# Optimization experiments

Hardware: AMD Instinct MI355X
Metric: run time of the kernel (lower is better)

The kernel has to match this reference:

```python
import jax, jax.numpy as jnp
import numpy as np
from jax import lax

NEG_INF = -1e30
GAP_OPEN = -5.0
GAP_EXTEND = -1.0
TEMP = 1.0


def setup_inputs() -> dict:
    key = jax.random.key(0)
    x = jax.random.normal(key, (2048, 2048), dtype=jnp.float32)
    return {"x": x}


def _sw_forward(x):
    xin = x[:-1, :-1]
    A, B = xin.shape  # static
    ar = jnp.arange(A - 1, -1, -1)[:, None]  # (A,1)
    br = jnp.arange(B)[None, :]              # (1,B)
    i = br - ar + (A - 1)                    # (A,B) diagonal index
    j = (ar + br) // 2                       # (A,B) position within diagonal
    n = A + B - 1
    m = (A + B) // 2
    # rotate score matrix into anti-diagonal (wavefront) layout
    smx = jnp.full((n, m), NEG_INF, dtype=x.dtype).at[i, j].set(xin)
    smo = (((jnp.arange(n) + A % 2) % 2)).astype(x.dtype)  # parity per diagonal

    right_pen = jnp.array([GAP_OPEN, GAP_EXTEND, GAP_OPEN], dtype=x.dtype)   # penalize_turns
    down_pen = jnp.array([GAP_OPEN, GAP_OPEN, GAP_EXTEND], dtype=x.dtype)

    def lse(a):
        return TEMP * jax.nn.logsumexp(a / TEMP, axis=-1)

    def step(carry, inp):
        h2, h1 = carry            # each (m,3)
        sx, so = inp              # (m,), scalar
        align = jnp.pad(h2, ((0, 0), (0, 1))) + sx[:, None]  # (m,4)
        right = so * jnp.pad(h1[:-1], ((1, 0), (0, 0)), constant_values=NEG_INF) + (1.0 - so) * h1
        down = so * h1 + (1.0 - so) * jnp.pad(h1[1:], ((0, 1), (0, 0)), constant_values=NEG_INF)
        right = (right + right_pen)[:, :2]  # restrict_turns
        down = down + down_pen
        h0 = jnp.stack([lse(align), lse(right), lse(down)], axis=-1)  # (m,3)
        return (h1, h0), h0

    carry0 = (jnp.full((m, 3), NEG_INF, dtype=x.dtype),
              jnp.full((m, 3), NEG_INF, dtype=x.dtype))
    _, results = lax.scan(step, carry0, (smx, smo))  # (n,m,3)

    hij = results[i, j]  # un-rotate -> (A,B,3)
    final = TEMP * jax.nn.logsumexp((hij + x[1:, 1:, None]) / TEMP)
    return final


def reference(x):
    return _sw_forward(x)
```

## Files before the change

kernel.cpp:

```cpp
#include <hip/hip_runtime.h>
#include <hip/hip_bf16.h>
#include <math.h>

#define NN 2048
#define TROWS 1040
#define NW 8
#define RPS 16
#define LN2 0.6931471805599453


__global__ void prep_kernel(const float* __restrict__ x, float* __restrict__ tab,
                            float* __restrict__ tabR) {
  const int c = blockIdx.x * 256 + threadIdx.x;
  const int t = blockIdx.y;
  tab[(size_t)t * NN + c] = __expf(x[(size_t)t * NN + c]);
  const int rr = 2048 - t, cc = 2048 - c;
  float v = 0.f;
  if (rr < 2048 && cc < 2048) v = __expf(x[(size_t)rr * NN + cc]);
  tabR[(size_t)t * NN + c] = v;
}

template<int MODE>
__global__ __launch_bounds__(NW * 64)
void sw2_kernel(const float* __restrict__ x, const float* __restrict__ tab,
                const float* __restrict__ tabR, float* __restrict__ arr,
                float* __restrict__ out) {
  const int tid  = threadIdx.x;
  const int lane = tid & 63;
  const int wv   = __builtin_amdgcn_readfirstlane(tid >> 6);
  const int c0   = (wv << 8) + lane * 4;

  __shared__ float2 E[2][NW + 1][RPS];
  __shared__ float  red[2][NW];
  __shared__ float  wsum[NW];

  for (int i = tid; i < 2 * (NW + 1) * RPS; i += NW * 64)
    ((float2*)E)[i] = make_float2(0.f, 0.f);
  __syncthreads();

  const float cGO = 0.006737946999085467f;
  const float cGE = 0.36787944117144233f;
  const float C4  = 0.01831563888873418f;
  const bool isL0 = (lane == 0), isL1 = (lane == 1), isL63 = (lane == 63);

  if (MODE == 0 || blockIdx.x == 0) {
    const int SPW   = (MODE == 0) ? 128 : 64;
    const int NSTEP = SPW + NW - 1;
    float s1_0=0.f,s1_1=0.f,s1_2=0.f,s1_3=0.f;
    float tg0=0.f,tg1=0.f,tg2=0.f,tg3=0.f;
    float yc0=0.f,yc1=0.f,yc2=0.f,yc3=0.f;
    float acc=0.f, one=1.f, tmx=0.f, escale=1.f, SinC=0.f;
    int Etot = 0;
    const float* src = ((MODE == 0) ? x : tab) + c0;
    float4 pfA = *(const float4*)(src);
    float4 pfB = *(const float4*)(src + NN);
    const float* pl = src + 2 * NN;
    int rown = 2;

    for (int s = 0; s < NSTEP; ++s) {
      const int pr = s & 1, cr = pr ^ 1;
      const bool act = (s >= wv) && (s < wv + SPW);
      if (act) {
        float prevEdx = 0.f;
        #pragma unroll
        for (int k = 0; k < RPS; ++k) {
          float4 ev;
          if (k & 1) { ev = pfB;
            if (MODE == 1) { pfB = *(const float4*)pl; pl += NN; }
            else { int rr = (rown < NN) ? rown : NN - 1; pfB = *(const float4*)(src + (size_t)rr * NN); rown++; }
          } else { ev = pfA;
            if (MODE == 1) { pfA = *(const float4*)pl; pl += NN; }
            else { int rr = (rown < NN) ? rown : NN - 1; pfA = *(const float4*)(src + (size_t)rr * NN); rown++; }
          }
          float ex0 = ev.x, ex1 = ev.y, ex2 = ev.z, ex3 = ev.w;
          if (MODE == 0) { ex0 = __expf(ex0); ex1 = __expf(ex1); ex2 = __expf(ex2); ex3 = __expf(ex3); }

          const float2 edc = E[cr][wv][k];
          const float Sr = (k == 0) ? SinC : prevEdx * escale;
          const float Xi = edc.y * escale;
          prevEdx = edc.x;

          float sh  = __shfl_up(s1_3, 1);
          float sd0 = isL0 ? Sr : sh;
          acc = fmaf(ex0, sd0,  acc);
          acc = fmaf(ex1, s1_0, acc);
          acc = fmaf(ex2, s1_1, acc);
          acc = fmaf(ex3, s1_2, acc);
          float M0 = ex0 * (sd0  + one);
          float M1 = ex1 * (s1_0 + one);
          float M2 = ex2 * (s1_1 + one);
          float M3 = ex3 * (s1_2 + one);

          float Q  = fmaf(cGE, fmaf(cGE, fmaf(cGE, M0, M1), M2), M3);
          float q1 = __shfl_up(Q, 1);
          float q2 = __shfl_up(Q, 2);
          q2 = isL1 ? Xi : q2;
          float X0 = fmaf(C4, q2, q1);
          X0 = isL0 ? Xi : X0;
          float X1 = fmaf(cGE, X0, M0);
          float X2 = fmaf(cGE, X1, M1);
          float X3 = fmaf(cGE, X2, M2);

          float T0 = fmaf(cGO, X0, M0);
          float T1 = fmaf(cGO, X1, M1);
          float T2 = fmaf(cGO, X2, M2);
          float T3 = fmaf(cGO, X3, M3);
          float Y0 = fmaf(cGE, yc0, tg0);
          float Y1 = fmaf(cGE, yc1, tg1);
          float Y2 = fmaf(cGE, yc2, tg2);
          float Y3 = fmaf(cGE, yc3, tg3);
          float S0 = T0 + Y0, S1n = T1 + Y1, S2n = T2 + Y2, S3n = T3 + Y3;
          tmx = fmaxf(tmx, fmaxf(fmaxf(S0, S1n), fmaxf(S2n, S3n)));
          tg0 = cGO * T0; tg1 = cGO * T1; tg2 = cGO * T2; tg3 = cGO * T3;
          yc0 = Y0; yc1 = Y1; yc2 = Y2; yc3 = Y3;
          s1_0 = S0; s1_1 = S1n; s1_2 = S2n; s1_3 = S3n;

          if (isL63) E[pr][wv + 1][k] = make_float2(S3n, fmaf(C4, X0, Q));
        }
        SinC = prevEdx * escale;
      }
      {
        float m = tmx;
        m = fmaxf(m, __shfl_xor(m, 1));  m = fmaxf(m, __shfl_xor(m, 2));
        m = fmaxf(m, __shfl_xor(m, 4));  m = fmaxf(m, __shfl_xor(m, 8));
        m = fmaxf(m, __shfl_xor(m, 16)); m = fmaxf(m, __shfl_xor(m, 32));
        if (lane == 0) red[pr][wv] = m;
      }
      __syncthreads();
      {
        float mm = red[pr][lane & (NW - 1)];
        mm = fmaxf(mm, __shfl_xor(mm, 1));
        mm = fmaxf(mm, __shfl_xor(mm, 2));
        mm = fmaxf(mm, __shfl_xor(mm, 4));
        tmx = 0.f; escale = 1.f;
        int e = (mm > 0.f) ? ilogbf(mm) : 0;
        if (e > 126) e = 126; if (e < -126) e = -126;
        if (e != 0) {
          const float c = ldexpf(1.f, -e);
          s1_0*=c; s1_1*=c; s1_2*=c; s1_3*=c;
          tg0*=c; tg1*=c; tg2*=c; tg3*=c;
          yc0*=c; yc1*=c; yc2*=c; yc3*=c;
          acc*=c; one*=c; SinC*=c;
          escale = c; Etot += e;
        }
      }
    }
    float ssum = acc;
    ssum += __shfl_xor(ssum, 1);  ssum += __shfl_xor(ssum, 2);
    ssum += __shfl_xor(ssum, 4);  ssum += __shfl_xor(ssum, 8);
    ssum += __shfl_xor(ssum, 16); ssum += __shfl_xor(ssum, 32);
    if (lane == 0) wsum[wv] = ssum;
    __syncthreads();
    if (MODE == 0) {
      if (tid == 0) {
        double tot = 0.0;
        #pragma unroll
        for (int k = 0; k < NW; ++k) tot += (double)wsum[k];
        out[0] = (float)(log(tot) + (double)Etot * LN2);
      }
    } else {
      *(float4*)(arr + c0)          = make_float4(s1_0, s1_1, s1_2, s1_3);
      *(float4*)(arr + NN + c0)     = make_float4(tg0, tg1, tg2, tg3);
      *(float4*)(arr + 2 * NN + c0) = make_float4(yc0, yc1, yc2, yc3);
      if (tid == 0) {
        float t = 0.f;
        #pragma unroll
        for (int k = 0; k < NW; ++k) t += wsum[k];
        arr[5 * NN + 0] = t;
        ((int*)(arr + 5 * NN))[2] = Etot;
      }
    }
  } else {
    float gM1_0=0.f,gM1_1=0.f,gM1_2=0.f,gM1_3=0.f;
    float gY1_0=0.f,gY1_1=0.f,gY1_2=0.f,gY1_3=0.f;
    float accB=0.f, one=1.f, tmx=0.f, escale=1.f, gMinC=0.f;
    int Etot = 0;
    const float* src = tabR + c0;
    float4 pfA = *(const float4*)(src);
    float4 pfB = *(const float4*)(src + NN);
    const float* pl = src + 2 * NN;

    const int NSTEPB = 64 + NW - 1 + 1;
    for (int s = 0; s < NSTEPB; ++s) {
      const int pr = s & 1, cr = pr ^ 1;
      const bool actM = (s >= wv) && (s < wv + 64);
      const bool actE = (s == wv + 64);
      if (actM) {
        float prevEdx = 0.f;
        #pragma unroll
        for (int k = 0; k < RPS; ++k) {
          float4 ev;
          if (k & 1) { ev = pfB; pfB = *(const float4*)pl; pl += NN; }
          else       { ev = pfA; pfA = *(const float4*)pl; pl += NN; }
          const float er0 = ev.x, er1 = ev.y, er2 = ev.z, er3 = ev.w;

          const float2 edc = E[cr][wv][k];
          const float gMdIn = (k == 0) ? gMinC : prevEdx * escale;
          const float Xi = edc.y * escale;
          prevEdx = edc.x;

          float gmh  = __shfl_up(gM1_3, 1);
          float gMd0 = isL0 ? gMdIn : gmh;
          float gMd1 = gM1_0, gMd2 = gM1_1, gMd3 = gM1_2;
          accB = fmaf(er0, gMd0, accB);
          accB = fmaf(er1, gMd1, accB);
          accB = fmaf(er2, gMd2, accB);
          accB = fmaf(er3, gMd3, accB);
          float a0 = er0 * (gMd0 + one);
          float a1 = er1 * (gMd1 + one);
          float a2 = er2 * (gMd2 + one);
          float a3 = er3 * (gMd3 + one);

          float gTs0 = fmaf(cGO, gY1_0, a0);
          float gTs1 = fmaf(cGO, gY1_1, a1);
          float gTs2 = fmaf(cGO, gY1_2, a2);
          float gTs3 = fmaf(cGO, gY1_3, a3);
          float gY0n = fmaf(cGE, gY1_0, a0);
          float gY1n = fmaf(cGE, gY1_1, a1);
          float gY2n = fmaf(cGE, gY1_2, a2);
          float gY3n = fmaf(cGE, gY1_3, a3);

          float Qg = fmaf(cGE, fmaf(cGE, fmaf(cGE, gTs0, gTs1), gTs2), gTs3);
          float q1 = __shfl_up(Qg, 1);
          float q2 = __shfl_up(Qg, 2);
          q2 = isL1 ? Xi : q2;
          float gXin = fmaf(C4, q2, q1);
          gXin = isL0 ? Xi : gXin;
          float gX0 = fmaf(cGE, gXin, gTs0);
          float gX1 = fmaf(cGE, gX0,  gTs1);
          float gX2 = fmaf(cGE, gX1,  gTs2);
          float gM0n = fmaf(cGO, gXin, gTs0);
          float gM1n = fmaf(cGO, gX0,  gTs1);
          float gM2n = fmaf(cGO, gX1,  gTs2);
          float gM3n = fmaf(cGO, gX2,  gTs3);

          tmx = fmaxf(tmx, fmaxf(fmaxf(gM0n, gM1n), fmaxf(gM2n, gM3n)));
          tmx = fmaxf(tmx, fmaxf(fmaxf(gY0n, gY1n), fmaxf(gY2n, gY3n)));
          gM1_0 = gM0n; gM1_1 = gM1n; gM1_2 = gM2n; gM1_3 = gM3n;
          gY1_0 = gY0n; gY1_1 = gY1n; gY1_2 = gY2n; gY1_3 = gY3n;

          if (isL63) E[pr][wv + 1][k] = make_float2(gM3n, fmaf(C4, gXin, Qg));
        }
        gMinC = prevEdx * escale;
      } else if (actE) {
        float gmh  = __shfl_up(gM1_3, 1);
        float gMd0 = isL0 ? gMinC : gmh;
        accB = fmaf(pfA.x, gMd0,  accB);
        accB = fmaf(pfA.y, gM1_0, accB);
        accB = fmaf(pfA.z, gM1_1, accB);
        accB = fmaf(pfA.w, gM1_2, accB);
      }
      {
        float m = tmx;
        m = fmaxf(m, __shfl_xor(m, 1));  m = fmaxf(m, __shfl_xor(m, 2));
        m = fmaxf(m, __shfl_xor(m, 4));  m = fmaxf(m, __shfl_xor(m, 8));
        m = fmaxf(m, __shfl_xor(m, 16)); m = fmaxf(m, __shfl_xor(m, 32));
        if (lane == 0) red[pr][wv] = m;
      }
      __syncthreads();
      {
        float mm = red[pr][lane & (NW - 1)];
        mm = fmaxf(mm, __shfl_xor(mm, 1));
        mm = fmaxf(mm, __shfl_xor(mm, 2));
        mm = fmaxf(mm, __shfl_xor(mm, 4));
        tmx = 0.f; escale = 1.f;
        int e = (mm > 0.f) ? ilogbf(mm) : 0;
        if (e > 126) e = 126; if (e < -126) e = -126;
        if (e != 0) {
          const float c = ldexpf(1.f, -e);
          gM1_0*=c; gM1_1*=c; gM1_2*=c; gM1_3*=c;
          gY1_0*=c; gY1_1*=c; gY1_2*=c; gY1_3*=c;
          accB*=c; one*=c; gMinC*=c;
          escale = c; Etot += e;
        }
      }
    }
    *(float4*)(arr + 3 * NN + (2044 - c0)) = make_float4(gM1_3, gM1_2, gM1_1, gM1_0);
    *(float4*)(arr + 4 * NN + (2044 - c0)) = make_float4(gY1_3, gY1_2, gY1_1, gY1_0);
    float ssum = accB;
    ssum += __shfl_xor(ssum, 1);  ssum += __shfl_xor(ssum, 2);
    ssum += __shfl_xor(ssum, 4);  ssum += __shfl_xor(ssum, 8);
    ssum += __shfl_xor(ssum, 16); ssum += __shfl_xor(ssum, 32);
    if (lane == 0) wsum[wv] = ssum;
    __syncthreads();
    if (tid == 0) {
      float t = 0.f;
      #pragma unroll
      for (int k = 0; k < NW; ++k) t += wsum[k];
      arr[5 * NN + 1] = t;
      ((int*)(arr + 5 * NN))[3] = Etot;
    }
  }
}

__global__ __launch_bounds__(1024)
void combine_kernel(const float* __restrict__ tab, const float* __restrict__ arr,
                    float* __restrict__ out) {
  __shared__ double sh01[16], sh0[16];
  const int tid = threadIdx.x, lane = tid & 63, wv = tid >> 6;
  const float cGE = 0.36787944117144233f;
  double t01 = 0.0, t0 = 0.0;
  for (int b = tid; b < NN; b += 1024) {
    const float S  = arr[b];
    const float tg = arr[NN + b];
    const float yc = arr[2 * NN + b];
    const float gY = arr[4 * NN + b];
    t01 += (double)gY * ((double)tg + (double)cGE * (double)yc);
    if (b < NN - 1) {
      const float es = tab[(size_t)1024 * NN + b + 1];
      const float gM = arr[3 * NN + b + 1];
      t01 += (double)es * (double)gM * (double)S;
      t0  += (double)es * (double)S;
    }
  }
  #pragma unroll
  for (int off = 1; off < 64; off <<= 1) {
    t01 += __shfl_xor(t01, off);
    t0  += __shfl_xor(t0, off);
  }
  if (lane == 0) { sh01[wv] = t01; sh0[wv] = t0; }
  __syncthreads();
  if (tid == 0) {
    double A01 = 0.0, A0 = 0.0;
    #pragma unroll
    for (int k = 0; k < 16; ++k) { A01 += sh01[k]; A0 += sh0[k]; }
    const float* resF = arr + 5 * NN;
    const float accTop = resF[0], accB = resF[1];
    const int E0 = ((const int*)resF)[2], E1 = ((const int*)resF)[3];
    A0 += (double)accTop;
    const double A1 = (double)accB;
    const long long e01 = (long long)E0 + (long long)E1;
    long long em = e01;
    if ((long long)E0 > em) em = E0;
    if ((long long)E1 > em) em = E1;
    const double tot = A01 * exp2((double)(e01 - em))
                     + A0  * exp2((double)((long long)E0 - em))
                     + A1  * exp2((double)((long long)E1 - em));
    out[0] = (float)(log(tot) + (double)em * LN2);
  }
}

extern "C" void kernel_launch(void* const* d_in, const int* in_sizes, int n_in,
                              void* d_out, int out_size, void* d_ws, size_t ws_size,
                              hipStream_t stream) {
  const float* x = (const float*)d_in[0];
  float* out = (float*)d_out;
  const size_t need = ((size_t)2 * TROWS * NN + 5 * NN + 16) * sizeof(float);
  if (ws_size >= need) {
    float* tab  = (float*)d_ws;
    float* tabR = tab + (size_t)TROWS * NN;
    float* arr  = tab + (size_t)2 * TROWS * NN;
    prep_kernel<<<dim3(NN / 256, TROWS), dim3(256), 0, stream>>>(x, tab, tabR);
    sw2_kernel<1><<<dim3(2), dim3(NW * 64), 0, stream>>>(x, tab, tabR, arr, out);
    combine_kernel<<<dim3(1), dim3(1024), 0, stream>>>(tab, arr, out);
  } else {
    sw2_kernel<0><<<dim3(1), dim3(NW * 64), 0, stream>>>(x, nullptr, nullptr, nullptr, out);
  }
}
```

Baseline: 285.8 us.

## Double rows per wavefront step and prefetch four rows ahead

Raises the rows processed per wave per pipeline step from 16 to 32, which halves the number of block-wide barriers and max-reduction/rescale rounds. The inner loop is restructured into groups of four rows with a four-deep register prefetch instead of two-deep. The cost is a longer pipeline fill/drain (each wave waits longer before starting), larger shared E buffers, and an inner loop that may no longer be fully unrolled, which could add overhead or register pressure.

Result: faster. 265.3 us, median of 2 (-7.2%).

```diff
diff --git a/kernel.cpp b/kernel.cpp
--- a/kernel.cpp
+++ b/kernel.cpp
@@ -5,7 +5,7 @@
 #define NN 2048
 #define TROWS 1040
 #define NW 8
-#define RPS 16
+#define RPS 32
 #define LN2 0.6931471805599453
 
 
@@ -44,7 +44,7 @@
   const bool isL0 = (lane == 0), isL1 = (lane == 1), isL63 = (lane == 63);
 
   if (MODE == 0 || blockIdx.x == 0) {
-    const int SPW   = (MODE == 0) ? 128 : 64;
+    const int SPW   = ((MODE == 0) ? 2048 : 1024) / RPS;
     const int NSTEP = SPW + NW - 1;
     float s1_0=0.f,s1_1=0.f,s1_2=0.f,s1_3=0.f;
     float tg0=0.f,tg1=0.f,tg2=0.f,tg3=0.f;
@@ -54,68 +54,87 @@
     const float* src = ((MODE == 0) ? x : tab) + c0;
     float4 pfA = *(const float4*)(src);
     float4 pfB = *(const float4*)(src + NN);
-    const float* pl = src + 2 * NN;
-    int rown = 2;
+    float4 pfC = *(const float4*)(src + 2 * NN);
+    float4 pfD = *(const float4*)(src + 3 * NN);
+    const float* pl = src + 4 * NN;
+    int rown = 4;
+
+    int cr_ = 0, pr_ = 0;
+    float prevEdx = 0.f;
+    auto rowF = [&](float4 ev, int k, bool first) {
+      float ex0 = ev.x, ex1 = ev.y, ex2 = ev.z, ex3 = ev.w;
+      if (MODE == 0) { ex0 = __expf(ex0); ex1 = __expf(ex1); ex2 = __expf(ex2); ex3 = __expf(ex3); }
+      const float2 edc = E[cr_][wv][k];
+      const float Sr = first ? SinC : prevEdx * escale;
+      const float Xi = edc.y * escale;
+      prevEdx = edc.x;
+
+      float sh  = __shfl_up(s1_3, 1);
+      float sd0 = isL0 ? Sr : sh;
+      acc = fmaf(ex0, sd0,  acc);
+      acc = fmaf(ex1, s1_0, acc);
+      acc = fmaf(ex2, s1_1, acc);
+      acc = fmaf(ex3, s1_2, acc);
+      float M0 = ex0 * (sd0  + one);
+      float M1 = ex1 * (s1_0 + one);
+      float M2 = ex2 * (s1_1 + one);
+      float M3 = ex3 * (s1_2 + one);
+
+      float Q  = fmaf(cGE, fmaf(cGE, fmaf(cGE, M0, M1), M2), M3);
+      float q1 = __shfl_up(Q, 1);
+      float q2 = __shfl_up(Q, 2);
+      q2 = isL1 ? Xi : q2;
+      float X0 = fmaf(C4, q2, q1);
+      X0 = isL0 ? Xi : X0;
+      float X1 = fmaf(cGE, X0, M0);
+      float X2 = fmaf(cGE, X1, M1);
+      float X3 = fmaf(cGE, X2, M2);
+
+      float T0 = fmaf(cGO, X0, M0);
+      float T1 = fmaf(cGO, X1, M1);
+      float T2 = fmaf(cGO, X2, M2);
+      float T3 = fmaf(cGO, X3, M3);
+      float Y0 = fmaf(cGE, yc0, tg0);
+      float Y1 = fmaf(cGE, yc1, tg1);
+      float Y2 = fmaf(cGE, yc2, tg2);
+      float Y3 = fmaf(cGE, yc3, tg3);
+      float S0 = T0 + Y0, S1n = T1 + Y1, S2n = T2 + Y2, S3n = T3 + Y3;
+      tmx = fmaxf(tmx, fmaxf(fmaxf(S0, S1n), fmaxf(S2n, S3n)));
+      tg0 = cGO * T0; tg1 = cGO * T1; tg2 = cGO * T2; tg3 = cGO * T3;
+      yc0 = Y0; yc1 = Y1; yc2 = Y2; yc3 = Y3;
+      s1_0 = S0; s1_1 = S1n; s1_2 = S2n; s1_3 = S3n;
+
+      if (isL63) E[pr_][wv + 1][k] = make_float2(S3n, fmaf(C4, X0, Q));
+    };
 
     for (int s = 0; s < NSTEP; ++s) {
-      const int pr = s & 1, cr = pr ^ 1;
+      pr_ = s & 1; cr_ = pr_ ^ 1;
       const bool act = (s >= wv) && (s < wv + SPW);
       if (act) {
-        float prevEdx = 0.f;
-        #pragma unroll
-        for (int k = 0; k < RPS; ++k) {
-          float4 ev;
-          if (k & 1) { ev = pfB;
-            if (MODE == 1) { pfB = *(const float4*)pl; pl += NN; }
-            else { int rr = (rown < NN) ? rown : NN - 1; pfB = *(const float4*)(src + (size_t)rr * NN); rown++; }
-          } else { ev = pfA;
-            if (MODE == 1) { pfA = *(const float4*)pl; pl += NN; }
-            else { int rr = (rown < NN) ? rown : NN - 1; pfA = *(const float4*)(src + (size_t)rr * NN); rown++; }
+        prevEdx = 0.f;
+        for (int kk = 0; kk < RPS / 4; ++kk) {
+          const int kb = kk << 2;
+          float4 e0 = pfA, e1 = pfB, e2 = pfC, e3 = pfD;
+          if (MODE == 1) {
+            pfA = *(const float4*)pl;          pl += NN;
+            pfB = *(const float4*)pl;          pl += NN;
+            pfC = *(const float4*)pl;          pl += NN;
+            pfD = *(const float4*)pl;          pl += NN;
+          } else {
+            int r0 = (rown     < NN) ? rown     : NN - 1;
+            int r1 = (rown + 1 < NN) ? rown + 1 : NN - 1;
+            int r2 = (rown + 2 < NN) ? rown + 2 : NN - 1;
+            int r3 = (rown + 3 < NN) ? rown + 3 : NN - 1;
+            pfA = *(const float4*)(src + (size_t)r0 * NN);
+            pfB = *(const float4*)(src + (size_t)r1 * NN);
+            pfC = *(const float4*)(src + (size_t)r2 * NN);
+            pfD = *(const float4*)(src + (size_t)r3 * NN);
+            rown += 4;
           }
-          float ex0 = ev.x, ex1 = ev.y, ex2 = ev.z, ex3 = ev.w;
-          if (MODE == 0) { ex0 = __expf(ex0); ex1 = __expf(ex1); ex2 = __expf(ex2); ex3 = __expf(ex3); }
-
-          const float2 edc = E[cr][wv][k];
-          const float Sr = (k == 0) ? SinC : prevEdx * escale;
-          const float Xi = edc.y * escale;
-          prevEdx = edc.x;
-
-          float sh  = __shfl_up(s1_3, 1);
-          float sd0 = isL0 ? Sr : sh;
-          acc = fmaf(ex0, sd0,  acc);
-          acc = fmaf(ex1, s1_0, acc);
-          acc = fmaf(ex2, s1_1, acc);
-          acc = fmaf(ex3, s1_2, acc);
-          float M0 = ex0 * (sd0  + one);
-          float M1 = ex1 * (s1_0 + one);
-          float M2 = ex2 * (s1_1 + one);
-          float M3 = ex3 * (s1_2 + one);
-
-          float Q  = fmaf(cGE, fmaf(cGE, fmaf(cGE, M0, M1), M2), M3);
-          float q1 = __shfl_up(Q, 1);
-          float q2 = __shfl_up(Q, 2);
-          q2 = isL1 ? Xi : q2;
-          float X0 = fmaf(C4, q2, q1);
-          X0 = isL0 ? Xi : X0;
-          float X1 = fmaf(cGE, X0, M0);
-          float X2 = fmaf(cGE, X1, M1);
-          float X3 = fmaf(cGE, X2, M2);
-
-          float T0 = fmaf(cGO, X0, M0);
-          float T1 = fmaf(cGO, X1, M1);
-          float T2 = fmaf(cGO, X2, M2);
-          float T3 = fmaf(cGO, X3, M3);
-          float Y0 = fmaf(cGE, yc0, tg0);
-          float Y1 = fmaf(cGE, yc1, tg1);
-          float Y2 = fmaf(cGE, yc2, tg2);
-          float Y3 = fmaf(cGE, yc3, tg3);
-          float S0 = T0 + Y0, S1n = T1 + Y1, S2n = T2 + Y2, S3n = T3 + Y3;
-          tmx = fmaxf(tmx, fmaxf(fmaxf(S0, S1n), fmaxf(S2n, S3n)));
-          tg0 = cGO * T0; tg1 = cGO * T1; tg2 = cGO * T2; tg3 = cGO * T3;
-          yc0 = Y0; yc1 = Y1; yc2 = Y2; yc3 = Y3;
-          s1_0 = S0; s1_1 = S1n; s1_2 = S2n; s1_3 = S3n;
-
-          if (isL63) E[pr][wv + 1][k] = make_float2(S3n, fmaf(C4, X0, Q));
+          rowF(e0, kb + 0, kk == 0);
+          rowF(e1, kb + 1, false);
+          rowF(e2, kb + 2, false);
+          rowF(e3, kb + 3, false);
         }
         SinC = prevEdx * escale;
       }
@@ -124,11 +143,11 @@
         m = fmaxf(m, __shfl_xor(m, 1));  m = fmaxf(m, __shfl_xor(m, 2));
         m = fmaxf(m, __shfl_xor(m, 4));  m = fmaxf(m, __shfl_xor(m, 8));
         m = fmaxf(m, __shfl_xor(m, 16)); m = fmaxf(m, __shfl_xor(m, 32));
-        if (lane == 0) red[pr][wv] = m;
+        if (lane == 0) red[pr_][wv] = m;
       }
       __syncthreads();
       {
-        float mm = red[pr][lane & (NW - 1)];
+        float mm = red[pr_][lane & (NW - 1)];
         mm = fmaxf(mm, __shfl_xor(mm, 1));
         mm = fmaxf(mm, __shfl_xor(mm, 2));
         mm = fmaxf(mm, __shfl_xor(mm, 4));
@@ -171,6 +190,7 @@
       }
     }
   } else {
+    const int SPWB = 1024 / RPS;
     float gM1_0=0.f,gM1_1=0.f,gM1_2=0.f,gM1_3=0.f;
     float gY1_0=0.f,gY1_1=0.f,gY1_2=0.f,gY1_3=0.f;
     float accB=0.f, one=1.f, tmx=0.f, escale=1.f, gMinC=0.f;
@@ -178,68 +198,80 @@
     const float* src = tabR + c0;
     float4 pfA = *(const float4*)(src);
     float4 pfB = *(const float4*)(src + NN);
-    const float* pl = src + 2 * NN;
-
-    const int NSTEPB = 64 + NW - 1 + 1;
+    float4 pfC = *(const float4*)(src + 2 * NN);
+    float4 pfD = *(const float4*)(src + 3 * NN);
+    const float* pl = src + 4 * NN;
+
+    int cr_ = 0, pr_ = 0;
+    float prevEdx = 0.f;
+    auto rowB = [&](float4 ev, int k, bool first) {
+      const float er0 = ev.x, er1 = ev.y, er2 = ev.z, er3 = ev.w;
+      const float2 edc = E[cr_][wv][k];
+      const float gMdIn = first ? gMinC : prevEdx * escale;
+      const float Xi = edc.y * escale;
+      prevEdx = edc.x;
+
+      float gmh  = __shfl_up(gM1_3, 1);
+      float gMd0 = isL0 ? gMdIn : gmh;
+      float gMd1 = gM1_0, gMd2 = gM1_1, gMd3 = gM1_2;
+      accB = fmaf(er0, gMd0, accB);
+      accB = fmaf(er1, gMd1, accB);
+      accB = fmaf(er2, gMd2, accB);
+      accB = fmaf(er3, gMd3, accB);
+      float a0 = er0 * (gMd0 + one);
+      float a1 = er1 * (gMd1 + one);
+      float a2 = er2 * (gMd2 + one);
+      float a3 = er3 * (gMd3 + one);
+
+      float gTs0 = fmaf(cGO, gY1_0, a0);
+      float gTs1 = fmaf(cGO, gY1_1, a1);
+      float gTs2 = fmaf(cGO, gY1_2, a2);
+      float gTs3 = fmaf(cGO, gY1_3, a3);
+      float gY0n = fmaf(cGE, gY1_0, a0);
+      float gY1n = fmaf(cGE, gY1_1, a1);
+      float gY2n = fmaf(cGE, gY1_2, a2);
+      float gY3n = fmaf(cGE, gY1_3, a3);
+
+      float Qg = fmaf(cGE, fmaf(cGE, fmaf(cGE, gTs0, gTs1), gTs2), gTs3);
+      float q1 = __shfl_up(Qg, 1);
+      float q2 = __shfl_up(Qg, 2);
+      q2 = isL1 ? Xi : q2;
+      float gXin = fmaf(C4, q2, q1);
+      gXin = isL0 ? Xi : gXin;
+      float gX0 = fmaf(cGE, gXin, gTs0);
+      float gX1 = fmaf(cGE, gX0,  gTs1);
+      float gX2 = fmaf(cGE, gX1,  gTs2);
+      float gM0n = fmaf(cGO, gXin, gTs0);
+      float gM1n = fmaf(cGO, gX0,  gTs1);
+      float gM2n = fmaf(cGO, gX1,  gTs2);
+      float gM3n = fmaf(cGO, gX2,  gTs3);
+
+      tmx = fmaxf(tmx, fmaxf(fmaxf(gM0n, gM1n), fmaxf(gM2n, gM3n)));
+      tmx = fmaxf(tmx, fmaxf(fmaxf(gY0n, gY1n), fmaxf(gY2n, gY3n)));
+      gM1_0 = gM0n; gM1_1 = gM1n; gM1_2 = gM2n; gM1_3 = gM3n;
+      gY1_0 = gY0n; gY1_1 = gY1n; gY1_2 = gY2n; gY1_3 = gY3n;
+
+      if (isL63) E[pr_][wv + 1][k] = make_float2(gM3n, fmaf(C4, gXin, Qg));
+    };
+
+    const int NSTEPB = SPWB + NW - 1 + 1;
     for (int s = 0; s < NSTEPB; ++s) {
-      const int pr = s & 1, cr = pr ^ 1;
-      const bool actM = (s >= wv) && (s < wv + 64);
-      const bool actE = (s == wv + 64);
+      pr_ = s & 1; cr_ = pr_ ^ 1;
+      const bool actM = (s >= wv) && (s < wv + SPWB);
+      const bool actE = (s == wv + SPWB);
       if (actM) {
-        float prevEdx = 0.f;
-        #pragma unroll
-        for (int k = 0; k < RPS; ++k) {
-          float4 ev;
-          if (k & 1) { ev = pfB; pfB = *(const float4*)pl; pl += NN; }
-          else       { ev = pfA; pfA = *(const float4*)pl; pl += NN; }
-          const float er0 = ev.x, er1 = ev.y, er2 = ev.z, er3 = ev.w;
-
-          const float2 edc = E[cr][wv][k];
-          const float gMdIn = (k == 0) ? gMinC : prevEdx * escale;
-          const float Xi = edc.y * escale;
-          prevEdx = edc.x;
-
-          float gmh  = __shfl_up(gM1_3, 1);
-          float gMd0 = isL0 ? gMdIn : gmh;
-          float gMd1 = gM1_0, gMd2 = gM1_1, gMd3 = gM1_2;
-          accB = fmaf(er0, gMd0, accB);
-          accB = fmaf(er1, gMd1, accB);
-          accB = fmaf(er2, gMd2, accB);
-          accB = fmaf(er3, gMd3, accB);
-          float a0 = er0 * (gMd0 + one);
-          float a1 = er1 * (gMd1 + one);
-          float a2 = er2 * (gMd2 + one);
-          float a3 = er3 * (gMd3 + one);
-
-          float gTs0 = fmaf(cGO, gY1_0, a0);
-          float gTs1 = fmaf(cGO, gY1_1, a1);
-          float gTs2 = fmaf(cGO, gY1_2, a2);
-          float gTs3 = fmaf(cGO, gY1_3, a3);
-          float gY0n = fmaf(cGE, gY1_0, a0);
-          float gY1n = fmaf(cGE, gY1_1, a1);
-          float gY2n = fmaf(cGE, gY1_2, a2);
-          float gY3n = fmaf(cGE, gY1_3, a3);
-
-          float Qg = fmaf(cGE, fmaf(cGE, fmaf(cGE, gTs0, gTs1), gTs2), gTs3);
-          float q1 = __shfl_up(Qg, 1);
-          float q2 = __shfl_up(Qg, 2);
-          q2 = isL1 ? Xi : q2;
-          float gXin = fmaf(C4, q2, q1);
-          gXin = isL0 ? Xi : gXin;
-          float gX0 = fmaf(cGE, gXin, gTs0);
-          float gX1 = fmaf(cGE, gX0,  gTs1);
-          float gX2 = fmaf(cGE, gX1,  gTs2);
-          float gM0n = fmaf(cGO, gXin, gTs0);
-          float gM1n = fmaf(cGO, gX0,  gTs1);
-          float gM2n = fmaf(cGO, gX1,  gTs2);
-          float gM3n = fmaf(cGO, gX2,  gTs3);
-
-          tmx = fmaxf(tmx, fmaxf(fmaxf(gM0n, gM1n), fmaxf(gM2n, gM3n)));
-          tmx = fmaxf(tmx, fmaxf(fmaxf(gY0n, gY1n), fmaxf(gY2n, gY3n)));
-          gM1_0 = gM0n; gM1_1 = gM1n; gM1_2 = gM2n; gM1_3 = gM3n;
-          gY1_0 = gY0n; gY1_1 = gY1n; gY1_2 = gY2n; gY1_3 = gY3n;
-
-          if (isL63) E[pr][wv + 1][k] = make_float2(gM3n, fmaf(C4, gXin, Qg));
+        prevEdx = 0.f;
+        for (int kk = 0; kk < RPS / 4; ++kk) {
+          const int kb = kk << 2;
+          float4 e0 = pfA, e1 = pfB, e2 = pfC, e3 = pfD;
+          pfA = *(const float4*)pl;            pl += NN;
+          pfB = *(const float4*)pl;            pl += NN;
+          pfC = *(const float4*)pl;            pl += NN;
+          pfD = *(const float4*)pl;            pl += NN;
+          rowB(e0, kb + 0, kk == 0);
+          rowB(e1, kb + 1, false);
+          rowB(e2, kb + 2, false);
+          rowB(e3, kb + 3, false);
         }
         gMinC = prevEdx * escale;
       } else if (actE) {
@@ -255,11 +287,11 @@
         m = fmaxf(m, __shfl_xor(m, 1));  m = fmaxf(m, __shfl_xor(m, 2));
         m = fmaxf(m, __shfl_xor(m, 4));  m = fmaxf(m, __shfl_xor(m, 8));
         m = fmaxf(m, __shfl_xor(m, 16)); m = fmaxf(m, __shfl_xor(m, 32));
-        if (lane == 0) red[pr][wv] = m;
+        if (lane == 0) red[pr_][wv] = m;
       }
       __syncthreads();
       {
-        float mm = red[pr][lane & (NW - 1)];
+        float mm = red[pr_][lane & (NW - 1)];
         mm = fmaxf(mm, __shfl_xor(mm, 1));
         mm = fmaxf(mm, __shfl_xor(mm, 2));
         mm = fmaxf(mm, __shfl_xor(mm, 4));
```
